# Performance work log

Measured on AMD Instinct MI355X. Metric: run time of the kernel, lower is better.

The kernel has to match this reference:

```python
import jax, jax.numpy as jnp
import numpy as np

B, T, H, W, C = 1, 16, 56, 56, 256
NH = 8
WS = (8, 7, 7)
SS = (4, 3, 3)
HID = 4 * C
N = WS[0] * WS[1] * WS[2]  # 392 tokens per window


def _rel_index(ws):
    wt, wh, ww = ws
    coords = np.stack(np.meshgrid(np.arange(wt), np.arange(wh), np.arange(ww), indexing='ij'))
    cf = coords.reshape(3, -1)
    rel = (cf[:, :, None] - cf[:, None, :]).transpose(1, 2, 0)
    rel[..., 0] += wt - 1
    rel[..., 1] += wh - 1
    rel[..., 2] += ww - 1
    rel[..., 0] *= (2 * wh - 1) * (2 * ww - 1)
    rel[..., 1] *= 2 * ww - 1
    return rel.sum(-1)  # (N, N) int


def _win_part_np(x, ws):
    b, t, h, w, c = x.shape
    x = x.reshape(b, t // ws[0], ws[0], h // ws[1], ws[1], w // ws[2], ws[2], c)
    return x.transpose(0, 1, 3, 5, 2, 4, 6, 7).reshape(-1, ws[0] * ws[1] * ws[2], c)


def _attn_mask(t, h, w, ws, ss):
    # static numpy construction of the shifted-window mask (nW, N, N)
    img = np.zeros((1, t, h, w, 1), dtype=np.float32)
    cnt = 0
    for d in (slice(-ws[0]), slice(-ws[0], -ss[0]), slice(-ss[0], None)):
        for hh in (slice(-ws[1]), slice(-ws[1], -ss[1]), slice(-ss[1], None)):
            for ww_ in (slice(-ws[2]), slice(-ws[2], -ss[2]), slice(-ss[2], None)):
                img[:, d, hh, ww_, :] = cnt
                cnt += 1
    mw = _win_part_np(img, ws).squeeze(-1)  # (nW, N)
    diff = mw[:, None, :] - mw[:, :, None]
    return np.where(diff != 0, np.float32(-100.0), np.float32(0.0))


_RPI = jnp.asarray(_rel_index(WS).reshape(-1))
_MASK = jnp.asarray(_attn_mask(T, H, W, WS, SS))  # (nW, N, N)


def _ln(x, g, b, eps=1e-5):
    mu = x.mean(-1, keepdims=True)
    var = ((x - mu) ** 2).mean(-1, keepdims=True)
    return (x - mu) * jax.lax.rsqrt(var + eps) * g + b


def _win_part(x, ws):
    b, t, h, w, c = x.shape
    x = x.reshape(b, t // ws[0], ws[0], h // ws[1], ws[1], w // ws[2], ws[2], c)
    return x.transpose(0, 1, 3, 5, 2, 4, 6, 7).reshape(-1, ws[0] * ws[1] * ws[2], c)


def _win_rev(win, ws, t, h, w):
    b = win.shape[0] // (t * h * w // (ws[0] * ws[1] * ws[2]))
    x = win.reshape(b, t // ws[0], h // ws[1], w // ws[2], ws[0], ws[1], ws[2], -1)
    return x.transpose(0, 1, 4, 2, 5, 3, 6, 7).reshape(b, t, h, w, -1)


def setup_inputs() -> dict:
    key = jax.random.key(0)
    ks = jax.random.split(key, 16)
    n_bias = (2 * WS[0] - 1) * (2 * WS[1] - 1) * (2 * WS[2] - 1)
    return {
        'x': jax.random.normal(ks[0], (B, T, H, W, C), jnp.float32),
        'norm1_g': jnp.ones((C,), jnp.float32),
        'norm1_b': jnp.zeros((C,), jnp.float32),
        'qkv_w': 0.02 * jax.random.normal(ks[1], (3 * C, C), jnp.float32),
        'qkv_b': jnp.zeros((3 * C,), jnp.float32),
        'rpb_table': 0.02 * jax.random.normal(ks[2], (n_bias, NH), jnp.float32),
        'proj_w': 0.02 * jax.random.normal(ks[3], (C, C), jnp.float32),
        'proj_b': jnp.zeros((C,), jnp.float32),
        'norm2_g': jnp.ones((C,), jnp.float32),
        'norm2_b': jnp.zeros((C,), jnp.float32),
        'fc1_w': 0.02 * jax.random.normal(ks[4], (HID, C), jnp.float32),
        'fc1_b': jnp.zeros((HID,), jnp.float32),
        'fc2_w': 0.02 * jax.random.normal(ks[5], (C, HID), jnp.float32),
        'fc2_b': jnp.zeros((C,), jnp.float32),
    }


def reference(x, norm1_g, norm1_b, qkv_w, qkv_b, rpb_table, proj_w, proj_b,
              norm2_g, norm2_b, fc1_w, fc1_b, fc2_w, fc2_b):
    hd = C // NH
    scale = hd ** -0.5
    shortcut = x
    h1 = _ln(x, norm1_g, norm1_b)
    # cyclic shift
    h1 = jnp.roll(h1, (-SS[0], -SS[1], -SS[2]), axis=(1, 2, 3))
    xw = _win_part(h1, WS)  # (B_, N, C)
    B_ = xw.shape[0]
    qkv = xw @ qkv_w.T + qkv_b  # (B_, N, 3C)
    qkv = qkv.reshape(B_, N, 3, NH, hd).transpose(2, 0, 3, 1, 4)
    q, k, v = qkv[0], qkv[1], qkv[2]  # (B_, NH, N, hd)
    attn = jnp.einsum('bhnd,bhmd->bhnm', q * scale, k)
    bias = rpb_table[_RPI].reshape(N, N, NH).transpose(2, 0, 1)  # (NH, N, N)
    attn = attn + bias[None]
    nW = _MASK.shape[0]
    attn = attn.reshape(B_ // nW, nW, NH, N, N) + _MASK[None, :, None]
    attn = jax.nn.softmax(attn, axis=-1).reshape(B_, NH, N, N)
    out = jnp.einsum('bhnm,bhmd->bhnd', attn, v).transpose(0, 2, 1, 3).reshape(B_, N, C)
    out = out @ proj_w.T + proj_b
    out = _win_rev(out, WS, T, H, W)
    out = jnp.roll(out, (SS[0], SS[1], SS[2]), axis=(1, 2, 3))
    x = shortcut + out
    # MLP with residual
    h2 = _ln(x, norm2_g, norm2_b)
    h2 = jax.nn.gelu(h2 @ fc1_w.T + fc1_b, approximate=False)
    return x + (h2 @ fc2_w.T + fc2_b)
```

## Files before the change

### kernel.cpp

```cpp
#include <hip/hip_runtime.h>
#include <hip/hip_bf16.h>
#include <cmath>

typedef unsigned short u16;
typedef unsigned int u32;

using bf16x8 = __attribute__((ext_vector_type(8))) short;
using f32x4  = __attribute__((ext_vector_type(4))) float;

__device__ __forceinline__ float b2f(u16 u) {
  union { u32 i; float f; } x; x.i = ((u32)u) << 16; return x.f;
}
__device__ __forceinline__ u16 f2b(float f) {
  union { float f; u32 i; } x; x.f = f;
  u32 r = x.i + 0x7fffu + ((x.i >> 16) & 1u);
  return (u16)(r >> 16);
}
__device__ __forceinline__ u32 cvtpk(float lo, float hi) {
  u32 r;
  asm("v_cvt_pk_bf16_f32 %0, %1, %2" : "=v"(r) : "v"(lo), "v"(hi));
  return r;
}
__device__ __forceinline__ float vexp2(float x) {
  float r;
  asm("v_exp_f32 %0, %1" : "=v"(r) : "v"(x));
  return r;
}
__device__ __forceinline__ void gload_lds16(const u16* g, u16* l) {
  __builtin_amdgcn_global_load_lds(
      (const __attribute__((address_space(1))) unsigned int*)g,
      (__attribute__((address_space(3))) unsigned int*)l, 16, 0, 0);
}

__global__ __launch_bounds__(256) void castw(const float* __restrict__ a,
                                             u16* __restrict__ o, int n) {
  int i = blockIdx.x * 256 + threadIdx.x;
  if (i < n) o[i] = f2b(a[i]);
}

__global__ __launch_bounds__(256) void bias_k(const float* __restrict__ rpb,
                                              u16* __restrict__ biasB,
                                              float* __restrict__ rowmax) {
  const int b = blockIdx.x;
  const int sl = b / 25, qt = b - sl * 25;
  const int head = sl & 7, cls = sl >> 3;
  const int tb = (cls >> 2) & 1, hb = (cls >> 1) & 1, wb = cls & 1;
  const int tid = threadIdx.x;
  const int lm = tid >> 4, kl = tid & 15;
  int q = qt * 16 + lm; if (q > 391) q = 391;
  const int ti = q / 49, rem = q - ti * 49, hi = rem / 7, wi = rem - hi * 7;
  const int cq = ti * 169 + hi * 13 + wi;
  const int rtq = tb ? (ti < 4 ? 1 : 2) : 0;
  const int rhq = hb ? (hi < 4 ? 1 : 2) : 0;
  const int rwq = wb ? (wi < 4 ? 1 : 2) : 0;
  const int labq = rtq * 9 + rhq * 3 + rwq;
  float mx = -3e38f;
  u16* ob = biasB + (size_t)b * 6400 + tid;
  for (int t = 0; t < 25; t++) {
    int k = t * 16 + kl;
    float v;
    if (k < 392) {
      int tk = k / 49, rk = k - tk * 49, hk = rk / 7, wk = rk - hk * 7;
      int ck = tk * 169 + hk * 13 + wk;
      float bv = rpb[(cq - ck + 1267) * 8 + head];
      int rt = tb ? (tk < 4 ? 1 : 2) : 0;
      int rh = hb ? (hk < 4 ? 1 : 2) : 0;
      int rw = wb ? (wk < 4 ? 1 : 2) : 0;
      if (rt * 9 + rh * 3 + rw != labq) bv -= 100.f;
      v = bv * 1.4426950408889634f;
      mx = fmaxf(mx, v);
    } else {
      v = -2081.f;
    }
    ob[t * 256] = f2b(v);
  }
  mx = fmaxf(mx, __shfl_xor(mx, 1, 64));
  mx = fmaxf(mx, __shfl_xor(mx, 2, 64));
  mx = fmaxf(mx, __shfl_xor(mx, 4, 64));
  mx = fmaxf(mx, __shfl_xor(mx, 8, 64));
  if (kl == 0) rowmax[sl * 392 + q] = mx;
}

__global__ __launch_bounds__(256) void ln_k(const float* __restrict__ src,
                                            const float* __restrict__ g,
                                            const float* __restrict__ b,
                                            u16* __restrict__ dst, int shifted) {
  const int wid = threadIdx.x >> 6, lane = threadIdx.x & 63;
  const int row = blockIdx.x * 4 + wid;
  int srow;
  if (shifted) {
    int widx = row / 392, n = row - widx * 392;
    int wt = widx >> 6, wh = (widx >> 3) & 7, ww = widx & 7;
    int ti = n / 49, rem = n - ti * 49, hi = rem / 7, wi = rem - hi * 7;
    int t = (wt * 8 + ti + 4) & 15;
    int h = wh * 7 + hi + 3; if (h >= 56) h -= 56;
    int w = ww * 7 + wi + 3; if (w >= 56) w -= 56;
    srow = (t * 56 + h) * 56 + w;
  } else {
    srow = row;
  }
  float4 v = *(const float4*)(src + (size_t)srow * 256 + lane * 4);
  float s = v.x + v.y + v.z + v.w;
  float sq = v.x * v.x + v.y * v.y + v.z * v.z + v.w * v.w;
  for (int o = 1; o < 64; o <<= 1) {
    s += __shfl_xor(s, o, 64);
    sq += __shfl_xor(sq, o, 64);
  }
  float mu = s * (1.0f / 256.0f);
  float rstd = rsqrtf(sq * (1.0f / 256.0f) - mu * mu + 1e-5f);
  float4 gg = *(const float4*)(g + lane * 4);
  float4 bb = *(const float4*)(b + lane * 4);
  ushort4 ov;
  ov.x = f2b((v.x - mu) * rstd * gg.x + bb.x);
  ov.y = f2b((v.y - mu) * rstd * gg.y + bb.y);
  ov.z = f2b((v.z - mu) * rstd * gg.z + bb.z);
  ov.w = f2b((v.w - mu) * rstd * gg.w + bb.w);
  *(ushort4*)(dst + (size_t)row * 256 + lane * 4) = ov;
}

template <int EPI, int TM>
__global__ __launch_bounds__(TM * 2) void gemm_k(const u16* __restrict__ A,
                                                 const u16* __restrict__ Bw,
                                                 int K, int tilesN,
                                                 const float* __restrict__ bias,
                                                 u16* __restrict__ outb,
                                                 float* __restrict__ outf,
                                                 const float* __restrict__ res,
                                                 float qscale) {
  constexpr int NW = TM / 32;
  constexpr int JA = TM * 8 / (NW * 64);
  constexpr int JB = 128 * 8 / (NW * 64);
  __shared__ __align__(16) u16 As[TM * 64];
  __shared__ __align__(16) u16 Bs[128 * 64];
  const int tid = threadIdx.x;
  const int swzb = ((int)blockIdx.x & 7) * ((int)gridDim.x >> 3) +
                   ((int)blockIdx.x >> 3);
  const int tm = swzb / tilesN, tn = swzb - tm * tilesN;
  const int wid = tid >> 6, lane = tid & 63;
  const int wm = wid >> 1, wn = wid & 1;
  const int lm = lane & 15, lk = lane >> 4;
  f32x4 acc[4][4] = {};
  const u16* Ap = A + (size_t)tm * TM * K;
  const u16* Bp = Bw + (size_t)tn * 128 * K;

  for (int k0 = 0; k0 < K; k0 += 64) {
    __syncthreads();
#pragma unroll
    for (int j = 0; j < JA; j++) {
      int s = (j * NW + wid) * 64 + lane;
      int r = s >> 3, c8 = (s & 7) ^ (r & 7);
      gload_lds16(Ap + (size_t)r * K + k0 + c8 * 8,
                  As + (size_t)(j * NW + wid) * 512);
    }
#pragma unroll
    for (int j = 0; j < JB; j++) {
      int s = (j * NW + wid) * 64 + lane;
      int r = s >> 3, c8 = (s & 7) ^ (r & 7);
      gload_lds16(Bp + (size_t)r * K + k0 + c8 * 8,
                  Bs + (size_t)(j * NW + wid) * 512);
    }
    __syncthreads();
#pragma unroll
    for (int ks = 0; ks < 2; ks++) {
      bf16x8 af[4], bfr[4];
#pragma unroll
      for (int f = 0; f < 4; f++) {
        int ra = wm * 64 + f * 16 + lm;
        int rb = wn * 64 + f * 16 + lm;
        af[f] = *(const bf16x8*)((const char*)As + ra * 128 +
                                 (((ks * 4 + lk) ^ (ra & 7)) << 4));
        bfr[f] = *(const bf16x8*)((const char*)Bs + rb * 128 +
                                  (((ks * 4 + lk) ^ (rb & 7)) << 4));
      }
#pragma unroll
      for (int fm = 0; fm < 4; fm++)
#pragma unroll
        for (int fn = 0; fn < 4; fn++)
          acc[fm][fn] = __builtin_amdgcn_mfma_f32_16x16x32_bf16(
              af[fm], bfr[fn], acc[fm][fn], 0, 0, 0);
    }
  }
  const int rbase = tm * TM + wm * 64, cbase = tn * 128 + wn * 64;
#pragma unroll
  for (int fm = 0; fm < 4; fm++) {
#pragma unroll
    for (int fn = 0; fn < 4; fn++) {
      const int col = cbase + fn * 16 + lm;
#pragma unroll
      for (int r = 0; r < 4; r++) {
        const int row = rbase + fm * 16 + lk * 4 + r;
        float v = acc[fm][fn][r] + bias[col];
        if (EPI == 0) {
          int s = col >> 8, rem = col & 255, head = rem >> 5, d = rem & 31;
          int widx = row / 392, n = row - widx * 392;
          size_t o;
          if (s == 2) {
            o = 25690112u + (((size_t)(widx * 8 + head)) * 32 + d) * 400 + n;
          } else {
            if (s == 0) v *= qscale;
            o = (size_t)s * 12845056u +
                (((size_t)(widx * 8 + head)) * 392 + n) * 32 + d;
          }
          outb[o] = f2b(v);
        } else if (EPI == 1) {
          int widx = row / 392, n = row - widx * 392;
          int wt = widx >> 6, wh = (widx >> 3) & 7, ww = widx & 7;
          int ti = n / 49, rem2 = n - ti * 49, hi = rem2 / 7, wi = rem2 - hi * 7;
          int t = (wt * 8 + ti + 4) & 15;
          int h = wh * 7 + hi + 3; if (h >= 56) h -= 56;
          int w = ww * 7 + wi + 3; if (w >= 56) w -= 56;
          size_t dr = ((size_t)(t * 56 + h)) * 56 + w;
          outf[dr * 256 + col] = res[dr * 256 + col] + v;
        } else if (EPI == 2) {
          float gv = 0.5f * v * (1.0f + erff(v * 0.70710678f));
          outb[(size_t)row * 1024 + col] = f2b(gv);
        } else {
          outf[(size_t)row * 256 + col] = res[(size_t)row * 256 + col] + v;
        }
      }
    }
  }
}

__global__ __launch_bounds__(256) void attn_k(const u16* __restrict__ qg,
                                              const u16* __restrict__ kg,
                                              const u16* __restrict__ vTg,
                                              const u16* __restrict__ biasB,
                                              const float* __restrict__ rowmax,
                                              u16* __restrict__ attno) {
  __shared__ __align__(16) char lds[60928];
  const int bid = blockIdx.x;
  const int widx = bid >> 3;
  const int tid = threadIdx.x;
  const size_t base = (size_t)bid * 12544;
  const int tb = (widx >> 6) & 1;
  const int hb = (((widx >> 3) & 7) == 7) ? 1 : 0;
  const int wb = ((widx & 7) == 7) ? 1 : 0;
  const int sl = (tb * 4 + hb * 2 + wb) * 8 + (bid & 7);
  const int VOFF = 25600;

#pragma unroll
  for (int i = 0; i < 6; i++) {
    int s = i * 256 + tid, r = s >> 2, cs = s & 3;
    gload_lds16(kg + base + r * 32 + ((cs ^ ((r >> 1) & 3)) << 3),
                (u16*)(lds + (size_t)(i * 256 + (tid & ~63)) * 16));
  }
  if (tid < 32) {
    int s = 1536 + tid, r = s >> 2, cs = s & 3;
    gload_lds16(kg + base + r * 32 + ((cs ^ ((r >> 1) & 3)) << 3),
                (u16*)(lds + (size_t)1536 * 16));
  }
  if (tid < 128) ((u32*)(lds + 25088))[tid] = 0u;
  {
    const u16* vsrc = vTg + (size_t)bid * 12800;
    for (int idx = tid; idx < 3200; idx += 256) {
      int d = idx / 100, c4 = idx - d * 100;
      *(ushort4*)(lds + VOFF + d * 848 + c4 * 8) =
          *(const ushort4*)(vsrc + d * 400 + c4 * 4);
    }
    for (int idx = tid; idx < 512; idx += 256) {
      int d = idx >> 4, e = idx & 15;
      *(u16*)(lds + VOFF + d * 848 + 800 + e * 2) = 0;
    }
  }
  __syncthreads();

  const int w = tid >> 6, lane = tid & 63;
  const int g = lane >> 4, lm = lane & 15;
  char* PqW = lds + 52736 + w * 2048 + lm * 128;
  const int swz = (lm & 7) << 4;
  const int kswz = ((lm >> 1) & 3);

  for (int qt = w; qt < 25; qt += 4) {
    const int q = qt * 16 + lm;
    const int qr = q < 391 ? q : 391;
    bf16x8 qf = *(const bf16x8*)(qg + base + (size_t)qr * 32 + g * 8);
    const u16* bp = biasB + ((size_t)(sl * 25 + qt) * 25) * 256 + lm * 16 + 4 * g;
    const float rmb = rowmax[sl * 392 + qr];
    f32x4 st[25];
#pragma unroll
    for (int t = 0; t < 25; t++) {
      ushort4 bb = *(const ushort4*)(bp + t * 256);
      f32x4 bacc = {b2f(bb.x), b2f(bb.y), b2f(bb.z), b2f(bb.w)};
      bf16x8 kf = *(const bf16x8*)(lds + (16 * t + lm) * 64 + ((g ^ kswz) << 4));
      st[t] = __builtin_amdgcn_mfma_f32_16x16x32_bf16(kf, qf, bacc, 0, 0, 0);
    }
    float m = -3e38f;
#pragma unroll
    for (int t = 0; t < 25; t++)
      m = fmaxf(m, fmaxf(fmaxf(st[t][0], st[t][1]), fmaxf(st[t][2], st[t][3])));
    m = fmaxf(m, __shfl_xor(m, 16, 64));
    m = fmaxf(m, __shfl_xor(m, 32, 64));
    m += rmb;

    float sum = 0.f;
    f32x4 oa0 = {0.f, 0.f, 0.f, 0.f}, oa1 = {0.f, 0.f, 0.f, 0.f};
#pragma unroll
    for (int p = 0; p < 6; p++) {
#pragma unroll
      for (int tl = 0; tl < 4; tl++) {
        int t = 4 * p + tl;
        float e0 = vexp2(st[t][0] - m), e1 = vexp2(st[t][1] - m);
        float e2 = vexp2(st[t][2] - m), e3 = vexp2(st[t][3] - m);
        sum += (e0 + e1) + (e2 + e3);
        uint2 pp;
        pp.x = cvtpk(e0, e1);
        pp.y = cvtpk(e2, e3);
        *(uint2*)(PqW + ((32 * tl + 8 * g) ^ swz)) = pp;
      }
      asm volatile("s_waitcnt lgkmcnt(0)" ::: "memory");
      __builtin_amdgcn_sched_barrier(0);
#pragma unroll
      for (int cl = 0; cl < 2; cl++) {
        int c = 2 * p + cl;
        bf16x8 pf = *(const bf16x8*)(PqW + ((64 * cl + 16 * g) ^ swz));
        const char* vrow = lds + VOFF + 64 * c + 16 * g;
        bf16x8 v0 = *(const bf16x8*)(vrow + lm * 848);
        bf16x8 v1 = *(const bf16x8*)(vrow + (16 + lm) * 848);
        oa0 = __builtin_amdgcn_mfma_f32_16x16x32_bf16(pf, v0, oa0, 0, 0, 0);
        oa1 = __builtin_amdgcn_mfma_f32_16x16x32_bf16(pf, v1, oa1, 0, 0, 0);
      }
      __builtin_amdgcn_sched_barrier(0);
    }
    {
      float e0 = vexp2(st[24][0] - m), e1 = vexp2(st[24][1] - m);
      float e2 = vexp2(st[24][2] - m), e3 = vexp2(st[24][3] - m);
      sum += (e0 + e1) + (e2 + e3);
      uint2 pp;
      pp.x = cvtpk(e0, e1);
      pp.y = cvtpk(e2, e3);
      *(uint2*)(PqW + ((8 * g) ^ swz)) = pp;
      uint2 zz; zz.x = 0u; zz.y = 0u;
      *(uint2*)(PqW + ((32 + 8 * g) ^ swz)) = zz;
      asm volatile("s_waitcnt lgkmcnt(0)" ::: "memory");
      __builtin_amdgcn_sched_barrier(0);
      bf16x8 pf = *(const bf16x8*)(PqW + ((16 * g) ^ swz));
      const char* vrow = lds + VOFF + 64 * 12 + 16 * g;
      bf16x8 v0 = *(const bf16x8*)(vrow + lm * 848);
      bf16x8 v1 = *(const bf16x8*)(vrow + (16 + lm) * 848);
      oa0 = __builtin_amdgcn_mfma_f32_16x16x32_bf16(pf, v0, oa0, 0, 0, 0);
      oa1 = __builtin_amdgcn_mfma_f32_16x16x32_bf16(pf, v1, oa1, 0, 0, 0);
      __builtin_amdgcn_sched_barrier(0);
    }
    sum += __shfl_xor(sum, 16, 64);
    sum += __shfl_xor(sum, 32, 64);
    const float inv = 1.f / sum;
#pragma unroll
    for (int r = 0; r < 4; r++) {
      int qq = qt * 16 + 4 * g + r;
      if (qq < 392) {
        u16* op = attno + ((size_t)(widx * 392 + qq)) * 256 + (bid & 7) * 32;
        op[lm] = f2b(oa0[r] * inv);
        op[16 + lm] = f2b(oa1[r] * inv);
      }
    }
  }
}

extern "C" void kernel_launch(void* const* d_in, const int* in_sizes, int n_in,
                              void* d_out, int out_size, void* d_ws,
                              size_t ws_size, hipStream_t stream) {
  const float* x     = (const float*)d_in[0];
  const float* n1g   = (const float*)d_in[1];
  const float* n1b   = (const float*)d_in[2];
  const float* qkvw  = (const float*)d_in[3];
  const float* qkvb  = (const float*)d_in[4];
  const float* rpb   = (const float*)d_in[5];
  const float* projw = (const float*)d_in[6];
  const float* projb = (const float*)d_in[7];
  const float* n2g   = (const float*)d_in[8];
  const float* n2b   = (const float*)d_in[9];
  const float* fc1w  = (const float*)d_in[10];
  const float* fc1b  = (const float*)d_in[11];
  const float* fc2w  = (const float*)d_in[12];
  const float* fc2b  = (const float*)d_in[13];

  const size_t NEED = 130547712;
  if (ws_size < NEED) return;

  char* ws = (char*)d_ws;
  u16* xw      = (u16*)(ws + 0LL);
  u16* qb      = (u16*)(ws + 25690112LL);
  u16* attno   = (u16*)(ws + 0LL);
  u16* hid     = (u16*)(ws + 0LL);
  u16* biasB   = (u16*)(ws + 103284736LL);
  float* rmx   = (float*)(ws + 123764736LL);
  u16* h2      = (u16*)(ws + 103284736LL);
  u16* wq      = (u16*)(ws + 128974848LL);
  u16* wp      = (u16*)(ws + 129368064LL);
  u16* w1      = (u16*)(ws + 129499136LL);
  u16* w2      = (u16*)(ws + 130023424LL);
  float* xres  = (float*)d_out;

  castw<<<768, 256, 0, stream>>>(qkvw, wq, 196608);
  castw<<<256, 256, 0, stream>>>(projw, wp, 65536);
  castw<<<1024, 256, 0, stream>>>(fc1w, w1, 262144);
  castw<<<1024, 256, 0, stream>>>(fc2w, w2, 262144);
  bias_k<<<1600, 256, 0, stream>>>(rpb, biasB, rmx);

  ln_k<<<12544, 256, 0, stream>>>(x, n1g, n1b, xw, 1);
  gemm_k<0, 256><<<196 * 6, 512, 0, stream>>>(
      xw, wq, 256, 6, qkvb, qb, nullptr, nullptr,
      0.17677669529663687f * 1.4426950408889634f);
  attn_k<<<1024, 256, 0, stream>>>(qb, qb + 12845056, qb + 2 * 12845056, biasB,
                                   rmx, attno);
  gemm_k<1, 128><<<392 * 2, 256, 0, stream>>>(attno, wp, 256, 2, projb,
                                              nullptr, xres, x, 0.f);
  ln_k<<<12544, 256, 0, stream>>>(xres, n2g, n2b, h2, 0);
  gemm_k<2, 256><<<196 * 8, 512, 0, stream>>>(h2, w1, 256, 8, fc1b, hid,
                                              nullptr, nullptr, 0.f);
  gemm_k<3, 128><<<392 * 2, 256, 0, stream>>>(hid, w2, 1024, 2, fc2b, nullptr,
                                              (float*)d_out, xres, 0.f);
}
```

Measured before the change: 350.1 us.

## Double-buffer GEMM LDS tiles with K=32 stages and merge weight cast kernels

Rewrites the GEMM main loop to use two LDS buffers with 32-wide K slices. The next slice's global-to-LDS load is issued before the MFMAs on the current slice, so memory latency overlaps with compute and only one barrier is needed per step. All GEMMs now use 256-row tiles with 512 threads, which halves the grid size for the proj and fc2 GEMMs. The four weight-cast launches are merged into one kernel. The trade-offs are lower occupancy from the larger tiles and fewer blocks for the N=256 GEMMs.

```diff
diff --git a/kernel.cpp b/kernel.cpp
--- a/kernel.cpp
+++ b/kernel.cpp
@@ -32,10 +32,19 @@
       (__attribute__((address_space(3))) unsigned int*)l, 16, 0, 0);
 }
 
-__global__ __launch_bounds__(256) void castw(const float* __restrict__ a,
-                                             u16* __restrict__ o, int n) {
+__global__ __launch_bounds__(256) void castw(const float* __restrict__ qkvw,
+                                             const float* __restrict__ projw,
+                                             const float* __restrict__ fc1w,
+                                             const float* __restrict__ fc2w,
+                                             u16* __restrict__ o) {
   int i = blockIdx.x * 256 + threadIdx.x;
-  if (i < n) o[i] = f2b(a[i]);
+  const float* src;
+  int off;
+  if (i < 196608)      { src = qkvw;  off = 0; }
+  else if (i < 262144) { src = projw; off = 196608; }
+  else if (i < 524288) { src = fc1w;  off = 262144; }
+  else                 { src = fc2w;  off = 524288; }
+  o[i] = f2b(src[i - off]);
 }
 
 __global__ __launch_bounds__(256) void bias_k(const float* __restrict__ rpb,
@@ -118,20 +127,17 @@
   *(ushort4*)(dst + (size_t)row * 256 + lane * 4) = ov;
 }
 
-template <int EPI, int TM>
-__global__ __launch_bounds__(TM * 2) void gemm_k(const u16* __restrict__ A,
-                                                 const u16* __restrict__ Bw,
-                                                 int K, int tilesN,
-                                                 const float* __restrict__ bias,
-                                                 u16* __restrict__ outb,
-                                                 float* __restrict__ outf,
-                                                 const float* __restrict__ res,
-                                                 float qscale) {
-  constexpr int NW = TM / 32;
-  constexpr int JA = TM * 8 / (NW * 64);
-  constexpr int JB = 128 * 8 / (NW * 64);
-  __shared__ __align__(16) u16 As[TM * 64];
-  __shared__ __align__(16) u16 Bs[128 * 64];
+template <int EPI>
+__global__ __launch_bounds__(512) void gemm_k(const u16* __restrict__ A,
+                                              const u16* __restrict__ Bw,
+                                              int K, int tilesN,
+                                              const float* __restrict__ bias,
+                                              u16* __restrict__ outb,
+                                              float* __restrict__ outf,
+                                              const float* __restrict__ res,
+                                              float qscale) {
+  __shared__ __align__(16) u16 As[2][256 * 32];
+  __shared__ __align__(16) u16 Bs[2][128 * 32];
   const int tid = threadIdx.x;
   const int swzb = ((int)blockIdx.x & 7) * ((int)gridDim.x >> 3) +
                    ((int)blockIdx.x >> 3);
@@ -140,47 +146,52 @@
   const int wm = wid >> 1, wn = wid & 1;
   const int lm = lane & 15, lk = lane >> 4;
   f32x4 acc[4][4] = {};
-  const u16* Ap = A + (size_t)tm * TM * K;
+  const u16* Ap = A + (size_t)tm * 256 * K;
   const u16* Bp = Bw + (size_t)tn * 128 * K;
 
-  for (int k0 = 0; k0 < K; k0 += 64) {
+  const int sA0 = wid * 128;
+  const int sB0 = wid * 64;
+  const int nt = K >> 5;
+
+#define STAGE(bufi, kk)                                                       \
+  {                                                                           \
+    int S = sA0 + lane, r = S >> 2, cs = S & 3;                               \
+    gload_lds16(Ap + (size_t)r * K + (kk) + ((cs ^ ((r >> 1) & 3)) << 3),     \
+                &As[bufi][sA0 * 8]);                                          \
+    S = sA0 + 64 + lane; r = S >> 2; cs = S & 3;                              \
+    gload_lds16(Ap + (size_t)r * K + (kk) + ((cs ^ ((r >> 1) & 3)) << 3),     \
+                &As[bufi][(sA0 + 64) * 8]);                                   \
+    S = sB0 + lane; r = S >> 2; cs = S & 3;                                   \
+    gload_lds16(Bp + (size_t)r * K + (kk) + ((cs ^ ((r >> 1) & 3)) << 3),     \
+                &Bs[bufi][sB0 * 8]);                                          \
+  }
+
+  STAGE(0, 0);
+  __syncthreads();
+  for (int t = 0; t < nt; t++) {
+    const int cur = t & 1;
+    if (t + 1 < nt) STAGE(cur ^ 1, (t + 1) << 5);
+    bf16x8 af[4], bfr[4];
+#pragma unroll
+    for (int f = 0; f < 4; f++) {
+      int ra = wm * 64 + f * 16 + lm;
+      int rb = wn * 64 + f * 16 + lm;
+      af[f] = *(const bf16x8*)((const char*)&As[cur][0] + ra * 64 +
+                               ((lk ^ ((ra >> 1) & 3)) << 4));
+      bfr[f] = *(const bf16x8*)((const char*)&Bs[cur][0] + rb * 64 +
+                                ((lk ^ ((rb >> 1) & 3)) << 4));
+    }
+#pragma unroll
+    for (int fm = 0; fm < 4; fm++)
+#pragma unroll
+      for (int fn = 0; fn < 4; fn++)
+        acc[fm][fn] = __builtin_amdgcn_mfma_f32_16x16x32_bf16(
+            af[fm], bfr[fn], acc[fm][fn], 0, 0, 0);
     __syncthreads();
-#pragma unroll
-    for (int j = 0; j < JA; j++) {
-      int s = (j * NW + wid) * 64 + lane;
-      int r = s >> 3, c8 = (s & 7) ^ (r & 7);
-      gload_lds16(Ap + (size_t)r * K + k0 + c8 * 8,
-                  As + (size_t)(j * NW + wid) * 512);
-    }
-#pragma unroll
-    for (int j = 0; j < JB; j++) {
-      int s = (j * NW + wid) * 64 + lane;
-      int r = s >> 3, c8 = (s & 7) ^ (r & 7);
-      gload_lds16(Bp + (size_t)r * K + k0 + c8 * 8,
-                  Bs + (size_t)(j * NW + wid) * 512);
-    }
-    __syncthreads();
-#pragma unroll
-    for (int ks = 0; ks < 2; ks++) {
-      bf16x8 af[4], bfr[4];
-#pragma unroll
-      for (int f = 0; f < 4; f++) {
-        int ra = wm * 64 + f * 16 + lm;
-        int rb = wn * 64 + f * 16 + lm;
-        af[f] = *(const bf16x8*)((const char*)As + ra * 128 +
-                                 (((ks * 4 + lk) ^ (ra & 7)) << 4));
-        bfr[f] = *(const bf16x8*)((const char*)Bs + rb * 128 +
-                                  (((ks * 4 + lk) ^ (rb & 7)) << 4));
-      }
-#pragma unroll
-      for (int fm = 0; fm < 4; fm++)
-#pragma unroll
-        for (int fn = 0; fn < 4; fn++)
-          acc[fm][fn] = __builtin_amdgcn_mfma_f32_16x16x32_bf16(
-              af[fm], bfr[fn], acc[fm][fn], 0, 0, 0);
-    }
-  }
-  const int rbase = tm * TM + wm * 64, cbase = tn * 128 + wn * 64;
+  }
+#undef STAGE
+
+  const int rbase = tm * 256 + wm * 64, cbase = tn * 128 + wn * 64;
 #pragma unroll
   for (int fm = 0; fm < 4; fm++) {
 #pragma unroll
@@ -392,23 +403,20 @@
   u16* w2      = (u16*)(ws + 130023424LL);
   float* xres  = (float*)d_out;
 
-  castw<<<768, 256, 0, stream>>>(qkvw, wq, 196608);
-  castw<<<256, 256, 0, stream>>>(projw, wp, 65536);
-  castw<<<1024, 256, 0, stream>>>(fc1w, w1, 262144);
-  castw<<<1024, 256, 0, stream>>>(fc2w, w2, 262144);
+  castw<<<3072, 256, 0, stream>>>(qkvw, projw, fc1w, fc2w, wq);
   bias_k<<<1600, 256, 0, stream>>>(rpb, biasB, rmx);
 
   ln_k<<<12544, 256, 0, stream>>>(x, n1g, n1b, xw, 1);
-  gemm_k<0, 256><<<196 * 6, 512, 0, stream>>>(
+  gemm_k<0><<<196 * 6, 512, 0, stream>>>(
       xw, wq, 256, 6, qkvb, qb, nullptr, nullptr,
       0.17677669529663687f * 1.4426950408889634f);
   attn_k<<<1024, 256, 0, stream>>>(qb, qb + 12845056, qb + 2 * 12845056, biasB,
                                    rmx, attno);
-  gemm_k<1, 128><<<392 * 2, 256, 0, stream>>>(attno, wp, 256, 2, projb,
-                                              nullptr, xres, x, 0.f);
+  gemm_k<1><<<196 * 2, 512, 0, stream>>>(attno, wp, 256, 2, projb, nullptr,
+                                         xres, x, 0.f);
   ln_k<<<12544, 256, 0, stream>>>(xres, n2g, n2b, h2, 0);
-  gemm_k<2, 256><<<196 * 8, 512, 0, stream>>>(h2, w1, 256, 8, fc1b, hid,
-                                              nullptr, nullptr, 0.f);
-  gemm_k<3, 128><<<392 * 2, 256, 0, stream>>>(hid, w2, 1024, 2, fc2b, nullptr,
-                                              (float*)d_out, xres, 0.f);
-}
+  gemm_k<2><<<196 * 8, 512, 0, stream>>>(h2, w1, 256, 8, fc1b, hid, nullptr,
+                                         nullptr, 0.f);
+  gemm_k<3><<<196 * 2, 512, 0, stream>>>(hid, w2, 1024, 2, fc2b, nullptr,
+                                         (float*)d_out, xres, 0.f);
+}
```

Measured after the change: 330.1 us. -5.7%, faster.
